# Kernel optimization log

Measured on AMD Instinct MI355X. Metric: run time of the kernel, lower is better.

## Reference

```python
import jax, jax.numpy as jnp
import numpy as np

B, N, K, F = 1, 50000, 16, 128
EPS = 1e-5

def _bn(h, gamma, beta):
    # BatchNorm1d in training mode: per-feature-channel stats over (batch, nodes)
    mean = jnp.mean(h, axis=(0, 1), keepdims=True)
    var = jnp.var(h, axis=(0, 1), keepdims=True)
    return (h - mean) * jax.lax.rsqrt(var + EPS) * gamma + beta

def _rgcn(h, neighbors, W, b):
    # pad one zero node row, gather K neighbors per node, flatten, linear
    h_pad = jnp.pad(h, ((0, 0), (0, 1), (0, 0)))           # [B, N+1, F]
    gathered = h_pad[:, neighbors]                          # [B, N, K, F]
    flat = gathered.reshape(h.shape[0], neighbors.shape[0], -1)  # [B, N, K*F]
    return jnp.einsum('bnk,ok->bno', flat, W) + b

def setup_inputs():
    key = jax.random.key(0)
    ks = jax.random.split(key, 10)
    x = jax.random.normal(ks[0], (B, N, F), jnp.float32)
    graph = jax.random.randint(ks[1], (N, K, 2), 0, N)
    gamma1 = 1.0 + 0.1 * jax.random.normal(ks[2], (F,), jnp.float32)
    beta1 = 0.1 * jax.random.normal(ks[3], (F,), jnp.float32)
    gamma2 = 1.0 + 0.1 * jax.random.normal(ks[4], (F,), jnp.float32)
    beta2 = 0.1 * jax.random.normal(ks[5], (F,), jnp.float32)
    s = 1.0 / np.sqrt(K * F)
    W1 = jax.random.uniform(ks[6], (F, K * F), jnp.float32, -s, s)
    b1 = jax.random.uniform(ks[7], (F,), jnp.float32, -s, s)
    W2 = jax.random.uniform(ks[8], (F, K * F), jnp.float32, -s, s)
    b2 = jax.random.uniform(ks[9], (F,), jnp.float32, -s, s)
    return {"x": x, "graph": graph, "gamma1": gamma1, "beta1": beta1,
            "W1": W1, "b1": b1, "gamma2": gamma2, "beta2": beta2,
            "W2": W2, "b2": b2}

def reference(x, graph, gamma1, beta1, W1, b1, gamma2, beta2, W2, b2):
    neighbors = graph[..., 1]                               # [N, K]
    out = jax.nn.gelu(_bn(x, gamma1, beta1), approximate=False)
    out = _rgcn(out, neighbors, W1, b1)                     # [B, N, F]
    out = jax.nn.gelu(_bn(out, gamma2, beta2), approximate=False)
    out = _rgcn(out, neighbors, W2, b2)                     # [B, N, F]
    return out + x
```

## Files before the change

kernel.cpp:

```cpp
#include <hip/hip_runtime.h>


#define NN  50000
#define NB  500
#define NPB 100

typedef __bf16 v8bf __attribute__((ext_vector_type(8)));
typedef unsigned short u8s __attribute__((ext_vector_type(8)));
typedef float  v4f  __attribute__((ext_vector_type(4)));
typedef float  vf2  __attribute__((ext_vector_type(2)));

__device__ __forceinline__ unsigned short f2bf(float f) {
  unsigned int u = __builtin_bit_cast(unsigned int, f);
  u += 0x7FFFu + ((u >> 16) & 1u);
  return (unsigned short)(u >> 16);
}
__device__ __forceinline__ float bf2f(unsigned short s) {
  unsigned int u = ((unsigned int)s) << 16;
  return __builtin_bit_cast(float, u);
}
__device__ __forceinline__ float gelu_f(float y) {
  return 0.5f * y * (1.0f + erff(y * 0.70710678118654752f));
}

__device__ __forceinline__ v8bf fp8x8_to_bf16x8(unsigned int lo, unsigned int hi) {
  vf2 f0 = __builtin_amdgcn_cvt_pk_f32_fp8((int)lo, false);
  vf2 f1 = __builtin_amdgcn_cvt_pk_f32_fp8((int)lo, true);
  vf2 f2 = __builtin_amdgcn_cvt_pk_f32_fp8((int)hi, false);
  vf2 f3 = __builtin_amdgcn_cvt_pk_f32_fp8((int)hi, true);
  unsigned int d0, d1, d2, d3;
  asm("v_cvt_pk_bf16_f32 %0, %1, %2" : "=v"(d0) : "v"(f0.x), "v"(f0.y));
  asm("v_cvt_pk_bf16_f32 %0, %1, %2" : "=v"(d1) : "v"(f1.x), "v"(f1.y));
  asm("v_cvt_pk_bf16_f32 %0, %1, %2" : "=v"(d2) : "v"(f2.x), "v"(f2.y));
  asm("v_cvt_pk_bf16_f32 %0, %1, %2" : "=v"(d3) : "v"(f3.x), "v"(f3.y));
  uint4 u = make_uint4(d0, d1, d2, d3);
  return __builtin_bit_cast(v8bf, u);
}

__global__ void wconv_kernel(const float* __restrict__ W1, const float* __restrict__ W2,
                             unsigned short* __restrict__ Wt1, unsigned short* __restrict__ Wt2) {
  int t = blockIdx.x * 256 + threadIdx.x;
  const bool is2 = (t >= 32768);
  const float* W = is2 ? W2 : W1;
  unsigned short* Wt = is2 ? Wt2 : Wt1;
  int r = t & 32767;
  int frag = r >> 6, lane = r & 63;
  int k4 = frag >> 3, c = frag & 7;
  int o  = c * 16 + (lane & 15);
  int lq = lane >> 4;
  int s_ = k4 >> 2, w_ = k4 & 3;
  int kd = s_ * 128 + (w_ >> 1) * 64 + lq * 16 + (w_ & 1) * 8;
  const float* src = W + o * 2048 + kd;
  unsigned short* dst = Wt + r * 8;
#pragma unroll
  for (int j = 0; j < 8; ++j) dst[j] = f2bf(src[j]);
}

__global__ void bn_stats_kernel(const float* __restrict__ x, float* __restrict__ part) {
  float s0=0,s1=0,s2=0,s3=0,q0=0,q1=0,q2=0,q3=0;
  for (int cb = blockIdx.x; cb < (NN*128/1024); cb += 256) {
    float4 v = reinterpret_cast<const float4*>(x)[cb * 256 + threadIdx.x];
    s0+=v.x; q0+=v.x*v.x; s1+=v.y; q1+=v.y*v.y;
    s2+=v.z; q2+=v.z*v.z; s3+=v.w; q3+=v.w*v.w;
  }
  __shared__ float ls[1024], lsq[1024];
  int fb = (threadIdx.x & 31) * 4;
  int sl = threadIdx.x >> 5;
  ls[sl*128+fb]   = s0; ls[sl*128+fb+1]  = s1; ls[sl*128+fb+2]  = s2; ls[sl*128+fb+3]  = s3;
  lsq[sl*128+fb]  = q0; lsq[sl*128+fb+1] = q1; lsq[sl*128+fb+2] = q2; lsq[sl*128+fb+3] = q3;
  __syncthreads();
  if (threadIdx.x < 128) {
    float S=0,Q=0;
#pragma unroll
    for (int s2i=0; s2i<8; ++s2i){ S += ls[s2i*128+threadIdx.x]; Q += lsq[s2i*128+threadIdx.x]; }
    part[blockIdx.x*256 + threadIdx.x]       = S;
    part[blockIdx.x*256 + 128 + threadIdx.x] = Q;
  }
}

__global__ __launch_bounds__(1024) void bn_reduce_kernel(
    const float* __restrict__ part, int nb,
    const float* __restrict__ gamma, const float* __restrict__ beta,
    float* __restrict__ scsh) {
  int f = threadIdx.x & 127;
  int g = threadIdx.x >> 7;
  float S = 0.f, Q = 0.f;
  for (int b = g; b < nb; b += 8) {
    S += part[b * 256 + f];
    Q += part[b * 256 + 128 + f];
  }
  __shared__ float ls[8][128], lq[8][128];
  ls[g][f] = S; lq[g][f] = Q;
  __syncthreads();
  if (threadIdx.x < 128) {
    float St = 0.f, Qt = 0.f;
#pragma unroll
    for (int i = 0; i < 8; ++i) { St += ls[i][f]; Qt += lq[i][f]; }
    float inv  = 1.0f / (float)NN;
    float mean = St * inv;
    float var  = fmaxf(Qt * inv - mean * mean, 0.0f);
    float sc   = gamma[f] * rsqrtf(var + 1e-5f);
    scsh[f]       = sc;
    scsh[128 + f] = beta[f] - mean * sc;
  }
}

__global__ void apply1_kernel(const float* __restrict__ x, const float* __restrict__ scsh,
                              unsigned int* __restrict__ h1) {
  int stride = gridDim.x * blockDim.x;
  for (int c = blockIdx.x * blockDim.x + threadIdx.x; c < NN*128/8; c += stride) {
    float4 v0 = reinterpret_cast<const float4*>(x)[c * 2];
    float4 v1 = reinterpret_cast<const float4*>(x)[c * 2 + 1];
    int f = (c * 8) & 127;
    float r[8] = {v0.x, v0.y, v0.z, v0.w, v1.x, v1.y, v1.z, v1.w};
#pragma unroll
    for (int j = 0; j < 8; ++j)
      r[j] = gelu_f(r[j] * scsh[f + j] + scsh[128 + f + j]);
    int lo = __builtin_amdgcn_cvt_pk_fp8_f32(r[0], r[1], 0,  false);
    lo     = __builtin_amdgcn_cvt_pk_fp8_f32(r[2], r[3], lo, true);
    int hi = __builtin_amdgcn_cvt_pk_fp8_f32(r[4], r[5], 0,  false);
    hi     = __builtin_amdgcn_cvt_pk_fp8_f32(r[6], r[7], hi, true);
    reinterpret_cast<uint2*>(h1)[c] = make_uint2((unsigned)lo, (unsigned)hi);
  }
}

__global__ void apply2_kernel(const unsigned short* __restrict__ t1,
                              const float* __restrict__ scsh,
                              unsigned int* __restrict__ h2) {
  int stride = gridDim.x * blockDim.x;
  for (int c = blockIdx.x * blockDim.x + threadIdx.x; c < NN*128/8; c += stride) {
    u8s v = reinterpret_cast<const u8s*>(t1)[c];
    int f = (c * 8) & 127;
    float r[8];
#pragma unroll
    for (int j = 0; j < 8; ++j)
      r[j] = gelu_f(bf2f((unsigned short)v[j]) * scsh[f + j] + scsh[128 + f + j]);
    int lo = __builtin_amdgcn_cvt_pk_fp8_f32(r[0], r[1], 0,  false);
    lo     = __builtin_amdgcn_cvt_pk_fp8_f32(r[2], r[3], lo, true);
    int hi = __builtin_amdgcn_cvt_pk_fp8_f32(r[4], r[5], 0,  false);
    hi     = __builtin_amdgcn_cvt_pk_fp8_f32(r[6], r[7], hi, true);
    reinterpret_cast<uint2*>(h2)[c] = make_uint2((unsigned)lo, (unsigned)hi);
  }
}

template<int MODE>
__global__ __launch_bounds__(256, 2) void rgcn_kernel(
    const unsigned char* __restrict__ h8,
    const unsigned short* __restrict__ Wt,
    const int* __restrict__ graph,
    const float* __restrict__ bias,
    const float* __restrict__ xres,
    float* __restrict__ outf,
    unsigned short* __restrict__ outb,
    float* __restrict__ part)
{
  __shared__ unsigned short bsm[32768];
  __shared__ float lds_s[4][128];
  __shared__ float lds_q[4][128];

  const int tid  = threadIdx.x;
  const int wv   = tid >> 6;
  const int lane = tid & 63;
  const int l15  = lane & 15;
  const int lq   = lane >> 4;
  const int nb0  = blockIdx.x * NPB;

  v4f acc[2][8];
#pragma unroll
  for (int rf = 0; rf < 2; ++rf)
#pragma unroll
    for (int c = 0; c < 8; ++c) acc[rf][c] = (v4f){0.f, 0.f, 0.f, 0.f};

  const int an0 = min(nb0 + wv * 32 + l15,      NN - 1);
  const int an1 = min(nb0 + wv * 32 + 16 + l15, NN - 1);

  int idx0[16], idx1[16];
  {
    const int4* g0 = reinterpret_cast<const int4*>(graph + an0 * 32);
    const int4* g1 = reinterpret_cast<const int4*>(graph + an1 * 32);
#pragma unroll
    for (int j = 0; j < 8; ++j) {
      int4 t0 = g0[j], t1v = g1[j];
      idx0[2*j]   = min(max(t0.y,  0), NN - 1) * 128;
      idx0[2*j+1] = min(max(t0.w,  0), NN - 1) * 128;
      idx1[2*j]   = min(max(t1v.y, 0), NN - 1) * 128;
      idx1[2*j+1] = min(max(t1v.w, 0), NN - 1) * 128;
    }
  }

  uint4 A0u[2][2][2], A1u[2][2][2];

#define LOADA2(buf_, p_) {                                                \
    _Pragma("unroll")                                                     \
    for (int sl = 0; sl < 2; ++sl) {                                      \
      const unsigned char* r0 = h8 + idx0[(p_) * 2 + sl] + lq * 16;       \
      const unsigned char* r1 = h8 + idx1[(p_) * 2 + sl] + lq * 16;       \
      A0u[buf_][sl][0] = *reinterpret_cast<const uint4*>(r0);             \
      A0u[buf_][sl][1] = *reinterpret_cast<const uint4*>(r0 + 64);        \
      A1u[buf_][sl][0] = *reinterpret_cast<const uint4*>(r1);             \
      A1u[buf_][sl][1] = *reinterpret_cast<const uint4*>(r1 + 64);        \
    }                                                                     \
  }

#define STAGE2(p_) {                                                          \
    const unsigned short* gsrc = Wt + (p_) * 32768 + wv * 8192 + lane * 8;    \
    unsigned short* ldst = &bsm[wv * 8192];                                   \
    _Pragma("unroll")                                                         \
    for (int i = 0; i < 16; ++i) {                                            \
      __builtin_amdgcn_global_load_lds(                                       \
        (const __attribute__((address_space(1))) void*)(gsrc + i * 512),      \
        (__attribute__((address_space(3))) void*)(ldst + i * 512),            \
        16, 0, 0);                                                            \
    }                                                                         \
  }

#define PHASE(p_) {                                                           \
    if ((p_) < 7) LOADA2(((p_) + 1) & 1, ((p_) + 1) & 7)                      \
    __builtin_amdgcn_sched_barrier(0);                                        \
    __builtin_amdgcn_s_setprio(1);                                            \
    {                                                                         \
      const int cur_ = (p_) & 1;                                              \
      _Pragma("unroll")                                                       \
      for (int sl = 0; sl < 2; ++sl) {                                        \
        _Pragma("unroll")                                                     \
        for (int w4 = 0; w4 < 4; ++w4) {                                      \
          uint4 u0 = A0u[cur_][sl][w4 >> 1];                                  \
          uint4 u1 = A1u[cur_][sl][w4 >> 1];                                  \
          v8bf a0v, a1v;                                                      \
          if ((w4 & 1) == 0) {                                                \
            a0v = fp8x8_to_bf16x8(u0.x, u0.y);                                \
            a1v = fp8x8_to_bf16x8(u1.x, u1.y);                                \
          } else {                                                            \
            a0v = fp8x8_to_bf16x8(u0.z, u0.w);                                \
            a1v = fp8x8_to_bf16x8(u1.z, u1.w);                                \
          }                                                                   \
          _Pragma("unroll")                                                   \
          for (int c = 0; c < 8; ++c) {                                       \
            v8bf b = *reinterpret_cast<const v8bf*>(                          \
                &bsm[sl * 16384 + (w4 * 8 + c) * 512 + lane * 8]);            \
            acc[0][c] = __builtin_amdgcn_mfma_f32_16x16x32_bf16(              \
                          a0v, b, acc[0][c], 0, 0, 0);                        \
            acc[1][c] = __builtin_amdgcn_mfma_f32_16x16x32_bf16(              \
                          a1v, b, acc[1][c], 0, 0, 0);                        \
          }                                                                   \
        }                                                                     \
      }                                                                       \
    }                                                                         \
    __builtin_amdgcn_s_setprio(0);                                            \
    __builtin_amdgcn_sched_barrier(0);                                        \
    __builtin_amdgcn_s_barrier();             \
    __builtin_amdgcn_sched_barrier(0);                                        \
    if ((p_) < 7) STAGE2(((p_) + 1) & 7)                                      \
    __syncthreads();                      \
  }

  STAGE2(0)
  LOADA2(0, 0)
  __syncthreads();

  PHASE(0)  PHASE(1)  PHASE(2)  PHASE(3)
  PHASE(4)  PHASE(5)  PHASE(6)  PHASE(7)
#undef PHASE
#undef LOADA2
#undef STAGE2

  if constexpr (MODE == 0) {
#pragma unroll
    for (int c = 0; c < 8; ++c) {
      float s = 0.f, q = 0.f;
#pragma unroll
      for (int rf = 0; rf < 2; ++rf) {
#pragma unroll
        for (int j = 0; j < 4; ++j) {
          int lrow = wv * 32 + rf * 16 + lq * 4 + j;
          float v  = acc[rf][c][j];
          if (lrow < NPB) { s += v; q += v * v; }
          bsm[lrow * 128 + c * 16 + l15] = f2bf(v);
        }
      }
      s += __shfl_xor(s, 16, 64); s += __shfl_xor(s, 32, 64);
      q += __shfl_xor(q, 16, 64); q += __shfl_xor(q, 32, 64);
      if (lq == 0) { lds_s[wv][c * 16 + l15] = s; lds_q[wv][c * 16 + l15] = q; }
    }
    __syncthreads();
    unsigned short* t1b = outb + nb0 * 128;
#pragma unroll
    for (int i = 0; i < 7; ++i) {
      int off = i * 2048 + tid * 8;
      if (off < NPB * 128) {
        *reinterpret_cast<u8s*>(t1b + off) =
            *reinterpret_cast<const u8s*>(&bsm[off]);
      }
    }
    if (tid < 128) {
      float S = lds_s[0][tid] + lds_s[1][tid] + lds_s[2][tid] + lds_s[3][tid];
      float Q = lds_q[0][tid] + lds_q[1][tid] + lds_q[2][tid] + lds_q[3][tid];
      part[blockIdx.x * 256 + tid]       = S;
      part[blockIdx.x * 256 + 128 + tid] = Q;
    }
  } else {
#pragma unroll
    for (int c = 0; c < 8; ++c) {
      float bv = bias[c * 16 + l15];
#pragma unroll
      for (int rf = 0; rf < 2; ++rf) {
#pragma unroll
        for (int j = 0; j < 4; ++j) {
          int node = nb0 + wv * 32 + rf * 16 + lq * 4 + j;
          if (node < nb0 + NPB) {
            int idx = node * 128 + c * 16 + l15;
            outf[idx] = acc[rf][c][j] + bv + xres[idx];
          }
        }
      }
    }
  }
}

extern "C" void kernel_launch(void* const* d_in, const int* in_sizes, int n_in,
                              void* d_out, int out_size, void* d_ws, size_t ws_size,
                              hipStream_t stream) {
  const float* x      = (const float*)d_in[0];
  const int*   graph  = (const int*)d_in[1];
  const float* gamma1 = (const float*)d_in[2];
  const float* beta1  = (const float*)d_in[3];
  const float* W1     = (const float*)d_in[4];
  const float* gamma2 = (const float*)d_in[6];
  const float* beta2  = (const float*)d_in[7];
  const float* W2     = (const float*)d_in[8];
  const float* b2     = (const float*)d_in[9];
  float* out = (float*)d_out;

  char* ws = (char*)d_ws;
  unsigned char*  h1  = (unsigned char*)(ws);
  unsigned short* t1  = (unsigned short*)(ws + 12800000);
  unsigned short* Wt1 = (unsigned short*)(ws + 25600000);
  unsigned short* Wt2 = (unsigned short*)(ws + 26124288);
  float* p1    = (float*)(ws + 26648576);
  float* p2    = (float*)(ws + 26910720);
  float* scsh1 = (float*)(ws + 27422720);
  float* scsh2 = (float*)(ws + 27423744);

  wconv_kernel<<<256, 256, 0, stream>>>(W1, W2, Wt1, Wt2);
  bn_stats_kernel<<<256, 256, 0, stream>>>(x, p1);
  bn_reduce_kernel<<<1, 1024, 0, stream>>>(p1, 256, gamma1, beta1, scsh1);
  apply1_kernel<<<2048, 256, 0, stream>>>(x, scsh1, (unsigned int*)h1);
  rgcn_kernel<0><<<NB, 256, 0, stream>>>(h1, Wt1, graph, nullptr, nullptr,
                                         nullptr, t1, p2);
  bn_reduce_kernel<<<1, 1024, 0, stream>>>(p2, NB, gamma2, beta2, scsh2);
  apply2_kernel<<<2048, 256, 0, stream>>>(t1, scsh2, (unsigned int*)h1);
  rgcn_kernel<1><<<NB, 256, 0, stream>>>(h1, Wt2, graph, b2, x,
                                         out, nullptr, nullptr);
}
```

Before: 203.6 us.

## Use single-wave blocks reading weights directly from global memory instead of LDS

Replaces the 4-wave, 256-thread RGCN blocks that staged weight slices into LDS with barriers by 64-thread blocks of 32 nodes each. Each wave loads the bf16 weight fragments straight from global/L2 and writes outputs and BN partial sums directly. This removes LDS staging and block-wide synchronization and gives many more blocks for occupancy. In exchange, weight reuse across waves moves from LDS to cache, so redundant global weight traffic rises. The output buffer is also reused as scratch for the partial sums.

Result: slower. 351.7 us (+72.7%).

```diff
diff --git a/kernel.cpp b/kernel.cpp
--- a/kernel.cpp
+++ b/kernel.cpp
@@ -2,8 +2,8 @@
 
 
 #define NN  50000
-#define NB  500
-#define NPB 100
+#define NB  1563
+#define NPB 32
 
 typedef __bf16 v8bf __attribute__((ext_vector_type(8)));
 typedef unsigned short u8s __attribute__((ext_vector_type(8)));
@@ -144,7 +144,7 @@
 }
 
 template<int MODE>
-__global__ __launch_bounds__(256, 2) void rgcn_kernel(
+__global__ __launch_bounds__(64) void rgcn_kernel(
     const unsigned char* __restrict__ h8,
     const unsigned short* __restrict__ Wt,
     const int* __restrict__ graph,
@@ -154,13 +154,7 @@
     unsigned short* __restrict__ outb,
     float* __restrict__ part)
 {
-  __shared__ unsigned short bsm[32768];
-  __shared__ float lds_s[4][128];
-  __shared__ float lds_q[4][128];
-
-  const int tid  = threadIdx.x;
-  const int wv   = tid >> 6;
-  const int lane = tid & 63;
+  const int lane = threadIdx.x & 63;
   const int l15  = lane & 15;
   const int lq   = lane >> 4;
   const int nb0  = blockIdx.x * NPB;
@@ -171,8 +165,8 @@
 #pragma unroll
     for (int c = 0; c < 8; ++c) acc[rf][c] = (v4f){0.f, 0.f, 0.f, 0.f};
 
-  const int an0 = min(nb0 + wv * 32 + l15,      NN - 1);
-  const int an1 = min(nb0 + wv * 32 + 16 + l15, NN - 1);
+  const int an0 = min(nb0 + l15,      NN - 1);
+  const int an1 = min(nb0 + 16 + l15, NN - 1);
 
   int idx0[16], idx1[16];
   {
@@ -188,81 +182,56 @@
     }
   }
 
-  uint4 A0u[2][2][2], A1u[2][2][2];
-
-#define LOADA2(buf_, p_) {                                                \
-    _Pragma("unroll")                                                     \
-    for (int sl = 0; sl < 2; ++sl) {                                      \
-      const unsigned char* r0 = h8 + idx0[(p_) * 2 + sl] + lq * 16;       \
-      const unsigned char* r1 = h8 + idx1[(p_) * 2 + sl] + lq * 16;       \
-      A0u[buf_][sl][0] = *reinterpret_cast<const uint4*>(r0);             \
-      A0u[buf_][sl][1] = *reinterpret_cast<const uint4*>(r0 + 64);        \
-      A1u[buf_][sl][0] = *reinterpret_cast<const uint4*>(r1);             \
-      A1u[buf_][sl][1] = *reinterpret_cast<const uint4*>(r1 + 64);        \
-    }                                                                     \
-  }
-
-#define STAGE2(p_) {                                                          \
-    const unsigned short* gsrc = Wt + (p_) * 32768 + wv * 8192 + lane * 8;    \
-    unsigned short* ldst = &bsm[wv * 8192];                                   \
-    _Pragma("unroll")                                                         \
-    for (int i = 0; i < 16; ++i) {                                            \
-      __builtin_amdgcn_global_load_lds(                                       \
-        (const __attribute__((address_space(1))) void*)(gsrc + i * 512),      \
-        (__attribute__((address_space(3))) void*)(ldst + i * 512),            \
-        16, 0, 0);                                                            \
-    }                                                                         \
-  }
-
-#define PHASE(p_) {                                                           \
-    if ((p_) < 7) LOADA2(((p_) + 1) & 1, ((p_) + 1) & 7)                      \
-    __builtin_amdgcn_sched_barrier(0);                                        \
-    __builtin_amdgcn_s_setprio(1);                                            \
+  uint4 A0u[2][2], A1u[2][2];
+
+#define LOADA(buf_, s_) {                                             \
+    const unsigned char* r0 = h8 + idx0[s_] + lq * 16;                \
+    const unsigned char* r1 = h8 + idx1[s_] + lq * 16;                \
+    A0u[buf_][0] = *reinterpret_cast<const uint4*>(r0);               \
+    A0u[buf_][1] = *reinterpret_cast<const uint4*>(r0 + 64);          \
+    A1u[buf_][0] = *reinterpret_cast<const uint4*>(r1);               \
+    A1u[buf_][1] = *reinterpret_cast<const uint4*>(r1 + 64);          \
+  }
+
+  const unsigned short* wlane = Wt + lane * 8;
+
+#define SLOT(s_) {                                                            \
+    if ((s_) < 15) LOADA(((s_) + 1) & 1, ((s_) + 1) & 15)                     \
     {                                                                         \
-      const int cur_ = (p_) & 1;                                              \
+      const int cur_ = (s_) & 1;                                              \
+      const unsigned short* wp = wlane + (s_) * 16384;                        \
       _Pragma("unroll")                                                       \
-      for (int sl = 0; sl < 2; ++sl) {                                        \
+      for (int w4 = 0; w4 < 4; ++w4) {                                        \
+        uint4 u0 = A0u[cur_][w4 >> 1];                                        \
+        uint4 u1 = A1u[cur_][w4 >> 1];                                        \
+        v8bf a0v, a1v;                                                        \
+        if ((w4 & 1) == 0) {                                                  \
+          a0v = fp8x8_to_bf16x8(u0.x, u0.y);                                  \
+          a1v = fp8x8_to_bf16x8(u1.x, u1.y);                                  \
+        } else {                                                              \
+          a0v = fp8x8_to_bf16x8(u0.z, u0.w);                                  \
+          a1v = fp8x8_to_bf16x8(u1.z, u1.w);                                  \
+        }                                                                     \
         _Pragma("unroll")                                                     \
-        for (int w4 = 0; w4 < 4; ++w4) {                                      \
-          uint4 u0 = A0u[cur_][sl][w4 >> 1];                                  \
-          uint4 u1 = A1u[cur_][sl][w4 >> 1];                                  \
-          v8bf a0v, a1v;                                                      \
-          if ((w4 & 1) == 0) {                                                \
-            a0v = fp8x8_to_bf16x8(u0.x, u0.y);                                \
-            a1v = fp8x8_to_bf16x8(u1.x, u1.y);                                \
-          } else {                                                            \
-            a0v = fp8x8_to_bf16x8(u0.z, u0.w);                                \
-            a1v = fp8x8_to_bf16x8(u1.z, u1.w);                                \
-          }                                                                   \
-          _Pragma("unroll")                                                   \
-          for (int c = 0; c < 8; ++c) {                                       \
-            v8bf b = *reinterpret_cast<const v8bf*>(                          \
-                &bsm[sl * 16384 + (w4 * 8 + c) * 512 + lane * 8]);            \
-            acc[0][c] = __builtin_amdgcn_mfma_f32_16x16x32_bf16(              \
-                          a0v, b, acc[0][c], 0, 0, 0);                        \
-            acc[1][c] = __builtin_amdgcn_mfma_f32_16x16x32_bf16(              \
-                          a1v, b, acc[1][c], 0, 0, 0);                        \
-          }                                                                   \
+        for (int c = 0; c < 8; ++c) {                                         \
+          v8bf b = *reinterpret_cast<const v8bf*>(wp + w4 * 4096 + c * 512);  \
+          acc[0][c] = __builtin_amdgcn_mfma_f32_16x16x32_bf16(                \
+                        a0v, b, acc[0][c], 0, 0, 0);                          \
+          acc[1][c] = __builtin_amdgcn_mfma_f32_16x16x32_bf16(                \
+                        a1v, b, acc[1][c], 0, 0, 0);                          \
         }                                                                     \
       }                                                                       \
     }                                                                         \
-    __builtin_amdgcn_s_setprio(0);                                            \
-    __builtin_amdgcn_sched_barrier(0);                                        \
-    __builtin_amdgcn_s_barrier();             \
-    __builtin_amdgcn_sched_barrier(0);                                        \
-    if ((p_) < 7) STAGE2(((p_) + 1) & 7)                                      \
-    __syncthreads();                      \
-  }
-
-  STAGE2(0)
-  LOADA2(0, 0)
-  __syncthreads();
-
-  PHASE(0)  PHASE(1)  PHASE(2)  PHASE(3)
-  PHASE(4)  PHASE(5)  PHASE(6)  PHASE(7)
-#undef PHASE
-#undef LOADA2
-#undef STAGE2
+  }
+
+  LOADA(0, 0)
+
+  SLOT(0)  SLOT(1)  SLOT(2)  SLOT(3)
+  SLOT(4)  SLOT(5)  SLOT(6)  SLOT(7)
+  SLOT(8)  SLOT(9)  SLOT(10) SLOT(11)
+  SLOT(12) SLOT(13) SLOT(14) SLOT(15)
+#undef SLOT
+#undef LOADA
 
   if constexpr (MODE == 0) {
 #pragma unroll
@@ -272,32 +241,21 @@
       for (int rf = 0; rf < 2; ++rf) {
 #pragma unroll
         for (int j = 0; j < 4; ++j) {
-          int lrow = wv * 32 + rf * 16 + lq * 4 + j;
+          int node = nb0 + rf * 16 + lq * 4 + j;
           float v  = acc[rf][c][j];
-          if (lrow < NPB) { s += v; q += v * v; }
-          bsm[lrow * 128 + c * 16 + l15] = f2bf(v);
+          if (node < NN) {
+            s += v; q += v * v;
+            outb[node * 128 + c * 16 + l15] = f2bf(v);
+          }
         }
       }
       s += __shfl_xor(s, 16, 64); s += __shfl_xor(s, 32, 64);
       q += __shfl_xor(q, 16, 64); q += __shfl_xor(q, 32, 64);
-      if (lq == 0) { lds_s[wv][c * 16 + l15] = s; lds_q[wv][c * 16 + l15] = q; }
-    }
-    __syncthreads();
-    unsigned short* t1b = outb + nb0 * 128;
-#pragma unroll
-    for (int i = 0; i < 7; ++i) {
-      int off = i * 2048 + tid * 8;
-      if (off < NPB * 128) {
-        *reinterpret_cast<u8s*>(t1b + off) =
-            *reinterpret_cast<const u8s*>(&bsm[off]);
+      if (lq == 0) {
+        part[blockIdx.x * 256 + c * 16 + l15]       = s;
+        part[blockIdx.x * 256 + 128 + c * 16 + l15] = q;
       }
     }
-    if (tid < 128) {
-      float S = lds_s[0][tid] + lds_s[1][tid] + lds_s[2][tid] + lds_s[3][tid];
-      float Q = lds_q[0][tid] + lds_q[1][tid] + lds_q[2][tid] + lds_q[3][tid];
-      part[blockIdx.x * 256 + tid]       = S;
-      part[blockIdx.x * 256 + 128 + tid] = Q;
-    }
   } else {
 #pragma unroll
     for (int c = 0; c < 8; ++c) {
@@ -306,8 +264,8 @@
       for (int rf = 0; rf < 2; ++rf) {
 #pragma unroll
         for (int j = 0; j < 4; ++j) {
-          int node = nb0 + wv * 32 + rf * 16 + lq * 4 + j;
-          if (node < nb0 + NPB) {
+          int node = nb0 + rf * 16 + lq * 4 + j;
+          if (node < NN) {
             int idx = node * 128 + c * 16 + l15;
             outf[idx] = acc[rf][c][j] + bv + xres[idx];
           }
@@ -337,18 +295,18 @@
   unsigned short* Wt1 = (unsigned short*)(ws + 25600000);
   unsigned short* Wt2 = (unsigned short*)(ws + 26124288);
   float* p1    = (float*)(ws + 26648576);
-  float* p2    = (float*)(ws + 26910720);
-  float* scsh1 = (float*)(ws + 27422720);
-  float* scsh2 = (float*)(ws + 27423744);
+  float* scsh1 = (float*)(ws + 26910720);
+  float* scsh2 = (float*)(ws + 26911744);
+  float* p2    = out;
 
   wconv_kernel<<<256, 256, 0, stream>>>(W1, W2, Wt1, Wt2);
   bn_stats_kernel<<<256, 256, 0, stream>>>(x, p1);
   bn_reduce_kernel<<<1, 1024, 0, stream>>>(p1, 256, gamma1, beta1, scsh1);
   apply1_kernel<<<2048, 256, 0, stream>>>(x, scsh1, (unsigned int*)h1);
-  rgcn_kernel<0><<<NB, 256, 0, stream>>>(h1, Wt1, graph, nullptr, nullptr,
-                                         nullptr, t1, p2);
+  rgcn_kernel<0><<<NB, 64, 0, stream>>>(h1, Wt1, graph, nullptr, nullptr,
+                                        nullptr, t1, p2);
   bn_reduce_kernel<<<1, 1024, 0, stream>>>(p2, NB, gamma2, beta2, scsh2);
   apply2_kernel<<<2048, 256, 0, stream>>>(t1, scsh2, (unsigned int*)h1);
-  rgcn_kernel<1><<<NB, 256, 0, stream>>>(h1, Wt2, graph, b2, x,
-                                         out, nullptr, nullptr);
-}
+  rgcn_kernel<1><<<NB, 64, 0, stream>>>(h1, Wt2, graph, b2, x,
+                                        out, nullptr, nullptr);
+}
```

## Fuse weight conversion into BN stats and BN finalize into apply kernels

Applied to the files above, without the earlier changes.

Merges the weight bf16 conversion into the first BN statistics kernel. Each apply kernel now reduces the per-block partial sums itself, so the single-block bn_reduce launches go away and the launch count drops from eight to five. The apply grids shrink from 2048 to 256 blocks so the redundant per-block reduction stays cheap, and the stage-2 partials are stored in the output buffer. The trade-off is repeated reduction work in every block (500 partials per block in stage 2) and fewer blocks to hide memory latency in the apply pass.

After: 250.0 us. 1.23x slower.

```diff
diff --git a/kernel.cpp b/kernel.cpp
--- a/kernel.cpp
+++ b/kernel.cpp
@@ -37,26 +37,10 @@
   return __builtin_bit_cast(v8bf, u);
 }
 
-__global__ void wconv_kernel(const float* __restrict__ W1, const float* __restrict__ W2,
-                             unsigned short* __restrict__ Wt1, unsigned short* __restrict__ Wt2) {
-  int t = blockIdx.x * 256 + threadIdx.x;
-  const bool is2 = (t >= 32768);
-  const float* W = is2 ? W2 : W1;
-  unsigned short* Wt = is2 ? Wt2 : Wt1;
-  int r = t & 32767;
-  int frag = r >> 6, lane = r & 63;
-  int k4 = frag >> 3, c = frag & 7;
-  int o  = c * 16 + (lane & 15);
-  int lq = lane >> 4;
-  int s_ = k4 >> 2, w_ = k4 & 3;
-  int kd = s_ * 128 + (w_ >> 1) * 64 + lq * 16 + (w_ & 1) * 8;
-  const float* src = W + o * 2048 + kd;
-  unsigned short* dst = Wt + r * 8;
-#pragma unroll
-  for (int j = 0; j < 8; ++j) dst[j] = f2bf(src[j]);
-}
-
-__global__ void bn_stats_kernel(const float* __restrict__ x, float* __restrict__ part) {
+__global__ __launch_bounds__(256) void prep_kernel(
+    const float* __restrict__ x, float* __restrict__ part,
+    const float* __restrict__ W1, const float* __restrict__ W2,
+    unsigned short* __restrict__ Wt1, unsigned short* __restrict__ Wt2) {
   float s0=0,s1=0,s2=0,s3=0,q0=0,q1=0,q2=0,q3=0;
   for (int cb = blockIdx.x; cb < (NN*128/1024); cb += 256) {
     float4 v = reinterpret_cast<const float4*>(x)[cb * 256 + threadIdx.x];
@@ -76,70 +60,78 @@
     part[blockIdx.x*256 + threadIdx.x]       = S;
     part[blockIdx.x*256 + 128 + threadIdx.x] = Q;
   }
-}
-
-__global__ __launch_bounds__(1024) void bn_reduce_kernel(
-    const float* __restrict__ part, int nb,
+  {
+    int t = blockIdx.x * 256 + threadIdx.x;
+    const bool is2 = (t >= 32768);
+    const float* W = is2 ? W2 : W1;
+    unsigned short* Wt = is2 ? Wt2 : Wt1;
+    int r = t & 32767;
+    int frag = r >> 6, lane = r & 63;
+    int k4 = frag >> 3, c = frag & 7;
+    int o  = c * 16 + (lane & 15);
+    int lq = lane >> 4;
+    int s_ = k4 >> 2, w_ = k4 & 3;
+    int kd = s_ * 128 + (w_ >> 1) * 64 + lq * 16 + (w_ & 1) * 8;
+    const float* src = W + o * 2048 + kd;
+    unsigned short* dst = Wt + r * 8;
+#pragma unroll
+    for (int j = 0; j < 8; ++j) dst[j] = f2bf(src[j]);
+  }
+}
+
+template<int SRC>
+__global__ __launch_bounds__(256) void apply_kernel(
+    const void* __restrict__ src, const float* __restrict__ part, int nb,
     const float* __restrict__ gamma, const float* __restrict__ beta,
-    float* __restrict__ scsh) {
-  int f = threadIdx.x & 127;
-  int g = threadIdx.x >> 7;
-  float S = 0.f, Q = 0.f;
-  for (int b = g; b < nb; b += 8) {
-    S += part[b * 256 + f];
-    Q += part[b * 256 + 128 + f];
-  }
-  __shared__ float ls[8][128], lq[8][128];
-  ls[g][f] = S; lq[g][f] = Q;
-  __syncthreads();
-  if (threadIdx.x < 128) {
-    float St = 0.f, Qt = 0.f;
-#pragma unroll
-    for (int i = 0; i < 8; ++i) { St += ls[i][f]; Qt += lq[i][f]; }
-    float inv  = 1.0f / (float)NN;
-    float mean = St * inv;
-    float var  = fmaxf(Qt * inv - mean * mean, 0.0f);
-    float sc   = gamma[f] * rsqrtf(var + 1e-5f);
-    scsh[f]       = sc;
-    scsh[128 + f] = beta[f] - mean * sc;
-  }
-}
-
-__global__ void apply1_kernel(const float* __restrict__ x, const float* __restrict__ scsh,
-                              unsigned int* __restrict__ h1) {
+    unsigned int* __restrict__ hout) {
+  __shared__ float sc_s[128], sh_s[128];
+  {
+    __shared__ float lsS[2][128], lsQ[2][128];
+    int f = threadIdx.x & 127;
+    int g = threadIdx.x >> 7;
+    float S = 0.f, Q = 0.f;
+    for (int b = g; b < nb; b += 2) {
+      S += part[b * 256 + f];
+      Q += part[b * 256 + 128 + f];
+    }
+    lsS[g][f] = S; lsQ[g][f] = Q;
+    __syncthreads();
+    if (threadIdx.x < 128) {
+      float St = lsS[0][f] + lsS[1][f];
+      float Qt = lsQ[0][f] + lsQ[1][f];
+      float inv  = 1.0f / (float)NN;
+      float mean = St * inv;
+      float var  = fmaxf(Qt * inv - mean * mean, 0.0f);
+      float sc   = gamma[f] * rsqrtf(var + 1e-5f);
+      sc_s[f] = sc;
+      sh_s[f] = beta[f] - mean * sc;
+    }
+    __syncthreads();
+  }
+  const float* xf = (const float*)src;
+  const unsigned short* tb = (const unsigned short*)src;
   int stride = gridDim.x * blockDim.x;
   for (int c = blockIdx.x * blockDim.x + threadIdx.x; c < NN*128/8; c += stride) {
-    float4 v0 = reinterpret_cast<const float4*>(x)[c * 2];
-    float4 v1 = reinterpret_cast<const float4*>(x)[c * 2 + 1];
     int f = (c * 8) & 127;
-    float r[8] = {v0.x, v0.y, v0.z, v0.w, v1.x, v1.y, v1.z, v1.w};
+    float r[8];
+    if constexpr (SRC == 0) {
+      float4 v0 = reinterpret_cast<const float4*>(xf)[c * 2];
+      float4 v1 = reinterpret_cast<const float4*>(xf)[c * 2 + 1];
+      r[0]=v0.x; r[1]=v0.y; r[2]=v0.z; r[3]=v0.w;
+      r[4]=v1.x; r[5]=v1.y; r[6]=v1.z; r[7]=v1.w;
+    } else {
+      u8s v = reinterpret_cast<const u8s*>(tb)[c];
+#pragma unroll
+      for (int j = 0; j < 8; ++j) r[j] = bf2f((unsigned short)v[j]);
+    }
 #pragma unroll
     for (int j = 0; j < 8; ++j)
-      r[j] = gelu_f(r[j] * scsh[f + j] + scsh[128 + f + j]);
+      r[j] = gelu_f(r[j] * sc_s[f + j] + sh_s[f + j]);
     int lo = __builtin_amdgcn_cvt_pk_fp8_f32(r[0], r[1], 0,  false);
     lo     = __builtin_amdgcn_cvt_pk_fp8_f32(r[2], r[3], lo, true);
     int hi = __builtin_amdgcn_cvt_pk_fp8_f32(r[4], r[5], 0,  false);
     hi     = __builtin_amdgcn_cvt_pk_fp8_f32(r[6], r[7], hi, true);
-    reinterpret_cast<uint2*>(h1)[c] = make_uint2((unsigned)lo, (unsigned)hi);
-  }
-}
-
-__global__ void apply2_kernel(const unsigned short* __restrict__ t1,
-                              const float* __restrict__ scsh,
-                              unsigned int* __restrict__ h2) {
-  int stride = gridDim.x * blockDim.x;
-  for (int c = blockIdx.x * blockDim.x + threadIdx.x; c < NN*128/8; c += stride) {
-    u8s v = reinterpret_cast<const u8s*>(t1)[c];
-    int f = (c * 8) & 127;
-    float r[8];
-#pragma unroll
-    for (int j = 0; j < 8; ++j)
-      r[j] = gelu_f(bf2f((unsigned short)v[j]) * scsh[f + j] + scsh[128 + f + j]);
-    int lo = __builtin_amdgcn_cvt_pk_fp8_f32(r[0], r[1], 0,  false);
-    lo     = __builtin_amdgcn_cvt_pk_fp8_f32(r[2], r[3], lo, true);
-    int hi = __builtin_amdgcn_cvt_pk_fp8_f32(r[4], r[5], 0,  false);
-    hi     = __builtin_amdgcn_cvt_pk_fp8_f32(r[6], r[7], hi, true);
-    reinterpret_cast<uint2*>(h2)[c] = make_uint2((unsigned)lo, (unsigned)hi);
+    reinterpret_cast<uint2*>(hout)[c] = make_uint2((unsigned)lo, (unsigned)hi);
   }
 }
 
@@ -337,18 +329,15 @@
   unsigned short* Wt1 = (unsigned short*)(ws + 25600000);
   unsigned short* Wt2 = (unsigned short*)(ws + 26124288);
   float* p1    = (float*)(ws + 26648576);
-  float* p2    = (float*)(ws + 26910720);
-  float* scsh1 = (float*)(ws + 27422720);
-  float* scsh2 = (float*)(ws + 27423744);
-
-  wconv_kernel<<<256, 256, 0, stream>>>(W1, W2, Wt1, Wt2);
-  bn_stats_kernel<<<256, 256, 0, stream>>>(x, p1);
-  bn_reduce_kernel<<<1, 1024, 0, stream>>>(p1, 256, gamma1, beta1, scsh1);
-  apply1_kernel<<<2048, 256, 0, stream>>>(x, scsh1, (unsigned int*)h1);
+  float* p2    = out;
+
+  prep_kernel<<<256, 256, 0, stream>>>(x, p1, W1, W2, Wt1, Wt2);
+  apply_kernel<0><<<256, 256, 0, stream>>>(x, p1, 256, gamma1, beta1,
+                                           (unsigned int*)h1);
   rgcn_kernel<0><<<NB, 256, 0, stream>>>(h1, Wt1, graph, nullptr, nullptr,
                                          nullptr, t1, p2);
-  bn_reduce_kernel<<<1, 1024, 0, stream>>>(p2, NB, gamma2, beta2, scsh2);
-  apply2_kernel<<<2048, 256, 0, stream>>>(t1, scsh2, (unsigned int*)h1);
+  apply_kernel<1><<<256, 256, 0, stream>>>(t1, p2, NB, gamma2, beta2,
+                                           (unsigned int*)h1);
   rgcn_kernel<1><<<NB, 256, 0, stream>>>(h1, Wt2, graph, b2, x,
                                          out, nullptr, nullptr);
 }
```
